# Kernel optimization log

Measured on AMD Instinct MI355X. Metric: run time of the kernel, lower is better.

The kernel has to match this reference:

```python
import jax, jax.numpy as jnp
import numpy as np

B, D, DOUT, R, H = 16384, 1024, 1024, 8, 16
DH = D // 2  # route hidden dim


def setup_inputs() -> dict:
    key = jax.random.key(0)
    ks = jax.random.split(key, 12)
    s = 0.02
    return {
        "x": jax.random.normal(ks[0], (B, D), dtype=jnp.float32),
        # nn.MultiheadAttention packed in_proj: [3D, D] (q,k,v stacked)
        "in_proj_w": jax.random.normal(ks[1], (3 * D, D), dtype=jnp.float32) * s,
        "in_proj_b": jax.random.normal(ks[2], (3 * D,), dtype=jnp.float32) * s,
        "out_proj_w": jax.random.normal(ks[3], (D, D), dtype=jnp.float32) * s,
        "out_proj_b": jax.random.normal(ks[4], (D,), dtype=jnp.float32) * s,
        # R expert MLPs, batched: Linear(D, D//2) -> ReLU -> Linear(D//2, DOUT)
        "W1": jax.random.normal(ks[5], (R, DH, D), dtype=jnp.float32) * s,
        "b1": jax.random.normal(ks[6], (R, DH), dtype=jnp.float32) * s,
        "W2": jax.random.normal(ks[7], (R, DOUT, DH), dtype=jnp.float32) * s,
        "b2": jax.random.normal(ks[8], (R, DOUT), dtype=jnp.float32) * s,
        # gate: Linear(D, R) + softmax
        "Wg": jax.random.normal(ks[9], (R, D), dtype=jnp.float32) * s,
        "bg": jax.random.normal(ks[10], (R,), dtype=jnp.float32) * s,
    }


def reference(x, in_proj_w, in_proj_b, out_proj_w, out_proj_b, W1, b1, W2, b2, Wg, bg):
    # --- MultiheadAttention over seq_len == 1 ---
    # softmax over a single key position is exactly 1 (for every head),
    # so attn_output == V; the Q/K projections provably do not affect the
    # output or any gradient (d softmax(single logit) = 0). Hence only the
    # V slice of the packed in_proj and the output projection matter.
    Wv = in_proj_w[2 * D:]          # [D, D]
    bv = in_proj_b[2 * D:]          # [D]
    v = x @ Wv.T + bv               # [B, D]
    attended = v @ out_proj_w.T + out_proj_b  # [B, D]

    # --- R small expert MLPs as one batched/grouped GEMM (dropout in eval mode = identity) ---
    h = jax.nn.relu(jnp.einsum('bd,rhd->brh', attended, W1) + b1)   # [B, R, DH]
    route_out = jnp.einsum('brh,roh->bro', h, W2) + b2              # [B, R, DOUT]

    # --- softmax gate over routes, computed from the ORIGINAL x ---
    gate = jax.nn.softmax(x @ Wg.T + bg, axis=-1)                   # [B, R]

    # gate-weighted sum over routes
    return jnp.einsum('bro,br->bo', route_out, gate)                # [B, DOUT]
```

## Files before the change

### kernel.cpp

```cpp
#include <hip/hip_runtime.h>
#include <hip/hip_bf16.h>
#include <cstdint>

typedef __hip_bfloat16 bf16;
typedef __attribute__((ext_vector_type(8))) short bfrag;
typedef __attribute__((ext_vector_type(4))) float facc;

#define B_    16384
#define D_    1024
#define DOUT_ 1024
#define R_    8
#define DH_   512
#define RH_   4096

#define BM 256
#define BN 256
#define BK 64

#define NXCD 8

#define AS1(p) ((const __attribute__((address_space(1))) void*)(p))
#define AS3(p) ((__attribute__((address_space(3))) void*)(p))

#define DSR(dst, addr, off) \
    asm volatile("ds_read_b128 %0, %1 offset:%c2" : "=v"(dst) : "v"(addr), "i"(off))

static __device__ __forceinline__ uint32_t pack2bf(float a, float b) {
    unsigned short ua = __builtin_bit_cast(unsigned short, __float2bfloat16(a));
    unsigned short ub = __builtin_bit_cast(unsigned short, __float2bfloat16(b));
    return (uint32_t)ua | ((uint32_t)ub << 16);
}

__global__ void k_cvt(const float* __restrict__ in, bf16* __restrict__ out, long n)
{
    long i = ((long)blockIdx.x * blockDim.x + threadIdx.x) * 4;
    if (i >= n) return;
    float4 v = *reinterpret_cast<const float4*>(in + i);
    uint2 o;
    o.x = pack2bf(v.x, v.y);
    o.y = pack2bf(v.z, v.w);
    *reinterpret_cast<uint2*>(out + i) = o;
}

__global__ void k_cvt_w2(const float* __restrict__ W2, bf16* __restrict__ out)
{
    int b = blockIdx.x;
    int r = b >> 10;
    int o = b & 1023;
    const float4* src = reinterpret_cast<const float4*>(W2 + ((long)r * DOUT_ + o) * DH_);
    bf16* dst = out + (long)o * RH_ + r * DH_;
    int t = threadIdx.x;
    float4 v = src[t];
    uint2 p;
    p.x = pack2bf(v.x, v.y);
    p.y = pack2bf(v.z, v.w);
    *reinterpret_cast<uint2*>(dst + t * 4) = p;
}

__global__ __launch_bounds__(256) void k_gate(const float* __restrict__ x,
                                              const float* __restrict__ Wg,
                                              const float* __restrict__ bg,
                                              float* __restrict__ gate)
{
    __shared__ float sWg[R_ * D_];
    __shared__ float sbg[R_];
    for (int i = threadIdx.x; i < R_ * D_ / 4; i += 256)
        reinterpret_cast<float4*>(sWg)[i] = reinterpret_cast<const float4*>(Wg)[i];
    if (threadIdx.x < R_) sbg[threadIdx.x] = bg[threadIdx.x];
    __syncthreads();

    const int lane = threadIdx.x & 63;
    const int wave = threadIdx.x >> 6;
    const int row  = blockIdx.x * 4 + wave;

    const float4* xr = reinterpret_cast<const float4*>(x + (long)row * D_);
    float s[R_] = {};
    #pragma unroll
    for (int c = 0; c < 4; ++c) {
        float4 xv = xr[lane + c * 64];
        #pragma unroll
        for (int r = 0; r < R_; ++r) {
            float4 wv = reinterpret_cast<const float4*>(sWg + r * D_)[lane + c * 64];
            s[r] += xv.x * wv.x + xv.y * wv.y + xv.z * wv.z + xv.w * wv.w;
        }
    }
    #pragma unroll
    for (int r = 0; r < R_; ++r) {
        float v = s[r];
        #pragma unroll
        for (int off = 32; off > 0; off >>= 1) v += __shfl_xor(v, off);
        s[r] = v + sbg[r];
    }
    float m = s[0];
    #pragma unroll
    for (int r = 1; r < R_; ++r) m = fmaxf(m, s[r]);
    float den = 0.f;
    #pragma unroll
    for (int r = 0; r < R_; ++r) { s[r] = __expf(s[r] - m); den += s[r]; }
    float inv = 1.f / den;
    if (lane < R_) gate[(long)row * R_ + lane] = s[lane] * inv;
}

#define MFMA_BF16 __builtin_amdgcn_mfma_f32_16x16x32_bf16

template <int EPI>
__global__ __launch_bounds__(512, 2)
void k_gemm(const bf16* __restrict__ A, const bf16* __restrict__ Bm,
            const float* __restrict__ bias, const float* __restrict__ gate,
            const float* __restrict__ b2v, void* __restrict__ Cout,
            int M, int N, int K, int gate_row0)
{
    __shared__ char lds[131072];

    const int tid  = threadIdx.x;
    const int lane = tid & 63;
    const int wave = tid >> 6;
    const int wr   = wave >> 2;
    const int wc   = wave & 3;

    const int nwg  = gridDim.x * gridDim.y;
    const int orig = blockIdx.y * gridDim.x + blockIdx.x;
    const int xcd  = orig % NXCD;
    const int q    = nwg / NXCD;
    const int rr   = nwg % NXCD;
    const int wgid = (xcd < rr ? xcd * (q + 1) : rr * (q + 1) + (xcd - rr) * q)
                   + orig / NXCD;
    const int bn0  = (wgid % gridDim.x) * BN;
    const int bm0  = (wgid / gridDim.x) * BM;

    const int lrow = lane & 15;
    const int kgrp = lane >> 4;

    const int s_colb  = ((tid & 7) * 16) ^ (((tid >> 3) & 7) << 4);
    const int s_row   = tid >> 3;
    const int lds_off = tid * 16;

    const long Kb   = (long)K * 2;
    const long r64  = 64 * Kb;
    const long r128 = 128 * Kb;
    const char* gA0 = (const char*)A  + (long)(bm0 + s_row) * Kb + s_colb;
    const char* gB0 = (const char*)Bm + (long)(bn0 + s_row) * Kb + s_colb;

    auto stageH = [&](int buf, int h, long kb) {
        char* ldst = lds + buf * 65536
                   + (h < 2 ? h * 16384 : 32768 + (h - 2) * 16384) + lds_off;
        const char* g = (h < 2 ? gA0 + h * r128 : gB0 + (h - 2) * r128) + kb;
        __builtin_amdgcn_global_load_lds(AS1(g),       AS3(ldst),        16, 0, 0);
        __builtin_amdgcn_global_load_lds(AS1(g + r64), AS3(ldst + 8192), 16, 0, 0);
    };

    const int swzk  = (lrow & 7) << 4;
    const int colK0 = (kgrp * 16) ^ swzk;
    const int colK1 = (kgrp * 16 + 64) ^ swzk;
    const uint32_t ldsbase = (uint32_t)(uintptr_t)AS3(lds);
    const uint32_t aA00 = ldsbase + (wr * 128 + lrow) * 128 + colK0;
    const uint32_t aA01 = ldsbase + (wr * 128 + lrow) * 128 + colK1;
    const uint32_t aB00 = ldsbase + 32768 + (wc * 64 + lrow) * 128 + colK0;
    const uint32_t aB01 = ldsbase + 32768 + (wc * 64 + lrow) * 128 + colK1;
    const uint32_t aA10 = aA00 + 65536, aA11 = aA01 + 65536;
    const uint32_t aB10 = aB00 + 65536, aB11 = aB01 + 65536;

    facc acc[8][4];
    #pragma unroll
    for (int m = 0; m < 8; ++m)
        #pragma unroll
        for (int n = 0; n < 4; ++n)
            acc[m][n] = facc{0.f, 0.f, 0.f, 0.f};

    const int NT = K / BK;

    stageH(0, 0, 0); stageH(0, 1, 0); stageH(0, 2, 0); stageH(0, 3, 0);
    stageH(1, 0, 128); stageH(1, 1, 128);
    asm volatile("s_waitcnt vmcnt(4)" ::: "memory");
    __builtin_amdgcn_s_barrier();

    bfrag aF[4][2], bLo[2][2], bHi[2][2];

    auto ktile = [&](int t, uint32_t A0, uint32_t A1, uint32_t Bb0, uint32_t Bb1,
                     int curbuf) {
        const int  nbuf = curbuf ^ 1;
        const long k1b  = (long)(t + 1) * 128;
        const long k2b  = (long)(t + 2) * 128;

        #pragma unroll
        for (int m = 0; m < 4; ++m) {
            DSR(aF[m][0], A0, m * 2048);
            DSR(aF[m][1], A1, m * 2048);
        }
        #pragma unroll
        for (int n = 0; n < 2; ++n) {
            DSR(bLo[n][0], Bb0, n * 2048);
            DSR(bLo[n][1], Bb1, n * 2048);
        }
        if (t + 1 < NT) stageH(nbuf, 2, k1b);
        __builtin_amdgcn_s_barrier();
        asm volatile("s_waitcnt lgkmcnt(0)" ::: "memory");
        __builtin_amdgcn_sched_barrier(0);
        __builtin_amdgcn_s_setprio(1);
        #pragma unroll
        for (int m = 0; m < 4; ++m)
            #pragma unroll
            for (int n = 0; n < 2; ++n) {
                acc[m][n] = MFMA_BF16(aF[m][0], bLo[n][0], acc[m][n], 0, 0, 0);
                acc[m][n] = MFMA_BF16(aF[m][1], bLo[n][1], acc[m][n], 0, 0, 0);
            }
        __builtin_amdgcn_s_setprio(0);
        __builtin_amdgcn_s_barrier();

        #pragma unroll
        for (int n = 0; n < 2; ++n) {
            DSR(bHi[n][0], Bb0, (2 + n) * 2048);
            DSR(bHi[n][1], Bb1, (2 + n) * 2048);
        }
        if (t + 1 < NT) stageH(nbuf, 3, k1b);
        __builtin_amdgcn_s_barrier();
        asm volatile("s_waitcnt lgkmcnt(0)" ::: "memory");
        __builtin_amdgcn_sched_barrier(0);
        __builtin_amdgcn_s_setprio(1);
        #pragma unroll
        for (int m = 0; m < 4; ++m)
            #pragma unroll
            for (int n = 0; n < 2; ++n) {
                acc[m][n + 2] = MFMA_BF16(aF[m][0], bHi[n][0], acc[m][n + 2], 0, 0, 0);
                acc[m][n + 2] = MFMA_BF16(aF[m][1], bHi[n][1], acc[m][n + 2], 0, 0, 0);
            }
        __builtin_amdgcn_s_setprio(0);
        __builtin_amdgcn_s_barrier();

        #pragma unroll
        for (int m = 0; m < 4; ++m) {
            DSR(aF[m][0], A0, (4 + m) * 2048);
            DSR(aF[m][1], A1, (4 + m) * 2048);
        }
        __builtin_amdgcn_s_barrier();
        asm volatile("s_waitcnt lgkmcnt(0)" ::: "memory");
        __builtin_amdgcn_sched_barrier(0);
        __builtin_amdgcn_s_setprio(1);
        #pragma unroll
        for (int m = 0; m < 4; ++m)
            #pragma unroll
            for (int n = 0; n < 2; ++n) {
                acc[m + 4][n + 2] = MFMA_BF16(aF[m][0], bHi[n][0], acc[m + 4][n + 2], 0, 0, 0);
                acc[m + 4][n + 2] = MFMA_BF16(aF[m][1], bHi[n][1], acc[m + 4][n + 2], 0, 0, 0);
            }
        __builtin_amdgcn_s_setprio(0);
        __builtin_amdgcn_s_barrier();

        if (t + 2 < NT) { stageH(curbuf, 0, k2b); stageH(curbuf, 1, k2b); }
        __builtin_amdgcn_s_barrier();
        __builtin_amdgcn_s_setprio(1);
        #pragma unroll
        for (int m = 0; m < 4; ++m)
            #pragma unroll
            for (int n = 0; n < 2; ++n) {
                acc[m + 4][n] = MFMA_BF16(aF[m][0], bLo[n][0], acc[m + 4][n], 0, 0, 0);
                acc[m + 4][n] = MFMA_BF16(aF[m][1], bLo[n][1], acc[m + 4][n], 0, 0, 0);
            }
        __builtin_amdgcn_s_setprio(0);
        if (t + 2 < NT)      asm volatile("s_waitcnt vmcnt(4)" ::: "memory");
        else if (t + 1 < NT) asm volatile("s_waitcnt vmcnt(0)" ::: "memory");
        __builtin_amdgcn_s_barrier();
    };

    for (int t = 0; t < NT; t += 2) {
        ktile(t,     aA00, aA01, aB00, aB01, 0);
        ktile(t + 1, aA10, aA11, aB10, aB11, 1);
    }

    if constexpr (EPI == 2) {
        float* Cf = reinterpret_cast<float*>(Cout);
        float b2c[4][R_];
        #pragma unroll
        for (int n = 0; n < 4; ++n) {
            const int col = bn0 + wc * 64 + n * 16 + lrow;
            #pragma unroll
            for (int r = 0; r < R_; ++r) b2c[n][r] = b2v[r * N + col];
        }
        #pragma unroll
        for (int m = 0; m < 8; ++m) {
            #pragma unroll
            for (int j = 0; j < 4; ++j) {
                const int row = bm0 + wr * 128 + m * 16 + kgrp * 4 + j;
                const float* g = gate + (long)(gate_row0 + row) * R_;
                float gv[R_];
                #pragma unroll
                for (int r = 0; r < R_; ++r) gv[r] = g[r];
                #pragma unroll
                for (int n = 0; n < 4; ++n) {
                    const int col = bn0 + wc * 64 + n * 16 + lrow;
                    float sv = acc[m][n][j];
                    #pragma unroll
                    for (int r = 0; r < R_; ++r) sv += gv[r] * b2c[n][r];
                    Cf[(long)row * N + col] = sv;
                }
            }
        }
    } else {
        bf16* Cb = reinterpret_cast<bf16*>(Cout);
        float bcol[4];
        #pragma unroll
        for (int n = 0; n < 4; ++n) bcol[n] = bias[bn0 + wc * 64 + n * 16 + lrow];
        #pragma unroll
        for (int m = 0; m < 8; ++m) {
            #pragma unroll
            for (int j = 0; j < 4; ++j) {
                const int row = bm0 + wr * 128 + m * 16 + kgrp * 4 + j;
                float gv[4];
                if constexpr (EPI == 1) {
                    #pragma unroll
                    for (int n = 0; n < 4; ++n) {
                        const int col = bn0 + wc * 64 + n * 16 + lrow;
                        gv[n] = gate[(long)(gate_row0 + row) * R_ + (col >> 9)];
                    }
                }
                #pragma unroll
                for (int n = 0; n < 4; ++n) {
                    const int col = bn0 + wc * 64 + n * 16 + lrow;
                    float v = acc[m][n][j] + bcol[n];
                    if constexpr (EPI == 1) v = fmaxf(v, 0.f) * gv[n];
                    Cb[(long)row * N + col] = __float2bfloat16(v);
                }
            }
        }
    }
}

extern "C" void kernel_launch(void* const* d_in, const int* in_sizes, int n_in,
                              void* d_out, int out_size, void* d_ws, size_t ws_size,
                              hipStream_t stream)
{
    const float* x   = (const float*)d_in[0];
    const float* ipw = (const float*)d_in[1];
    const float* ipb = (const float*)d_in[2];
    const float* opw = (const float*)d_in[3];
    const float* opb = (const float*)d_in[4];
    const float* W1  = (const float*)d_in[5];
    const float* b1  = (const float*)d_in[6];
    const float* W2  = (const float*)d_in[7];
    const float* b2  = (const float*)d_in[8];
    const float* Wg  = (const float*)d_in[9];
    const float* bg  = (const float*)d_in[10];
    float* out = (float*)d_out;

    char* ws = (char*)d_ws;
    size_t off = 0;
    auto alloc = [&](size_t bytes) -> void* {
        void* p = ws + off;
        off += (bytes + 255) & ~(size_t)255;
        return p;
    };

    bf16* xb   = (bf16*)alloc((size_t)B_ * D_ * 2);
    bf16* vb   = (bf16*)alloc((size_t)B_ * D_ * 2);
    bf16* Wvb  = (bf16*)alloc((size_t)D_ * D_ * 2);
    bf16* Wob  = (bf16*)alloc((size_t)D_ * D_ * 2);
    bf16* W1b  = (bf16*)alloc((size_t)RH_ * D_ * 2);
    bf16* W2b  = (bf16*)alloc((size_t)DOUT_ * RH_ * 2);
    float* gate = (float*)alloc((size_t)B_ * R_ * 4);

    int mc = B_;
    while (off + (size_t)mc * RH_ * 2 > ws_size && mc > 1024) mc >>= 1;
    bf16* hb = (bf16*)alloc((size_t)mc * RH_ * 2);
    bf16* ab = xb;

    k_cvt<<<(B_ * D_) / 1024, 256, 0, stream>>>(x, xb, (long)B_ * D_);
    k_cvt<<<(D_ * D_) / 1024, 256, 0, stream>>>(ipw + (size_t)2 * D_ * D_, Wvb, (long)D_ * D_);
    k_cvt<<<(D_ * D_) / 1024, 256, 0, stream>>>(opw, Wob, (long)D_ * D_);
    k_cvt<<<(RH_ * D_) / 1024, 256, 0, stream>>>(W1, W1b, (long)RH_ * D_);
    k_cvt_w2<<<R_ * DOUT_, 128, 0, stream>>>(W2, W2b);

    k_gate<<<B_ / 4, 256, 0, stream>>>(x, Wg, bg, gate);

    k_gemm<0><<<dim3(D_ / BN, B_ / BM), 512, 0, stream>>>(
        xb, Wvb, ipb + 2 * D_, nullptr, nullptr, vb, B_, D_, D_, 0);

    k_gemm<0><<<dim3(D_ / BN, B_ / BM), 512, 0, stream>>>(
        vb, Wob, opb, nullptr, nullptr, ab, B_, D_, D_, 0);

    for (int m0 = 0; m0 < B_; m0 += mc) {
        k_gemm<1><<<dim3(RH_ / BN, mc / BM), 512, 0, stream>>>(
            ab + (size_t)m0 * D_, W1b, b1, gate, nullptr, hb, mc, RH_, D_, m0);
        k_gemm<2><<<dim3(DOUT_ / BN, mc / BM), 512, 0, stream>>>(
            hb, W2b, nullptr, gate, b2, out + (size_t)m0 * DOUT_, mc, DOUT_, RH_, m0);
    }
}
```

Before: 385.7 us.

## Software-pipeline LDS fragment reads across k-tiles with double-buffered B fragments

```diff
diff --git a/kernel.cpp b/kernel.cpp
--- a/kernel.cpp
+++ b/kernel.cpp
@@ -169,30 +169,31 @@
 
     const int NT = K / BK;
 
+    bfrag aF[4][2];
+    bfrag bHi[2][2];
+    bfrag bLoE[2][2];
+    bfrag bLoO[2][2];
+
     stageH(0, 0, 0); stageH(0, 1, 0); stageH(0, 2, 0); stageH(0, 3, 0);
     stageH(1, 0, 128); stageH(1, 1, 128);
     asm volatile("s_waitcnt vmcnt(4)" ::: "memory");
     __builtin_amdgcn_s_barrier();
-
-    bfrag aF[4][2], bLo[2][2], bHi[2][2];
-
-    auto ktile = [&](int t, uint32_t A0, uint32_t A1, uint32_t Bb0, uint32_t Bb1,
-                     int curbuf) {
-        const int  nbuf = curbuf ^ 1;
-        const long k1b  = (long)(t + 1) * 128;
-        const long k2b  = (long)(t + 2) * 128;
-
-        #pragma unroll
-        for (int m = 0; m < 4; ++m) {
-            DSR(aF[m][0], A0, m * 2048);
-            DSR(aF[m][1], A1, m * 2048);
-        }
-        #pragma unroll
-        for (int n = 0; n < 2; ++n) {
-            DSR(bLo[n][0], Bb0, n * 2048);
-            DSR(bLo[n][1], Bb1, n * 2048);
-        }
-        if (t + 1 < NT) stageH(nbuf, 2, k1b);
+    #pragma unroll
+    for (int m = 0; m < 4; ++m) { DSR(aF[m][0], aA00, 0 * 2048 + 0); DSR(aF[m][1], aA01, 0); }
+    #pragma unroll
+    for (int m = 0; m < 4; ++m) { DSR(aF[m][0], aA00, m * 2048); DSR(aF[m][1], aA01, m * 2048); }
+    #pragma unroll
+    for (int n = 0; n < 2; ++n) { DSR(bLoE[n][0], aB00, n * 2048); DSR(bLoE[n][1], aB01, n * 2048); }
+
+    auto ktile = [&](int t, int curbuf,
+                     uint32_t A0c, uint32_t A1c, uint32_t B0c, uint32_t B1c,
+                     uint32_t A0n, uint32_t A1n, uint32_t B0n, uint32_t B1n,
+                     bfrag (&bLoC)[2][2], bfrag (&bLoN)[2][2]) {
+        const long k1b = (long)(t + 1) * 128;
+        const long k2b = (long)(t + 2) * 128;
+        const int  nb  = curbuf ^ 1;
+
+        if (t + 1 < NT) stageH(nb, 2, k1b);
         __builtin_amdgcn_s_barrier();
         asm volatile("s_waitcnt lgkmcnt(0)" ::: "memory");
         __builtin_amdgcn_sched_barrier(0);
@@ -201,18 +202,18 @@
         for (int m = 0; m < 4; ++m)
             #pragma unroll
             for (int n = 0; n < 2; ++n) {
-                acc[m][n] = MFMA_BF16(aF[m][0], bLo[n][0], acc[m][n], 0, 0, 0);
-                acc[m][n] = MFMA_BF16(aF[m][1], bLo[n][1], acc[m][n], 0, 0, 0);
+                acc[m][n] = MFMA_BF16(aF[m][0], bLoC[n][0], acc[m][n], 0, 0, 0);
+                acc[m][n] = MFMA_BF16(aF[m][1], bLoC[n][1], acc[m][n], 0, 0, 0);
             }
         __builtin_amdgcn_s_setprio(0);
-        __builtin_amdgcn_s_barrier();
-
         #pragma unroll
         for (int n = 0; n < 2; ++n) {
-            DSR(bHi[n][0], Bb0, (2 + n) * 2048);
-            DSR(bHi[n][1], Bb1, (2 + n) * 2048);
-        }
-        if (t + 1 < NT) stageH(nbuf, 3, k1b);
+            DSR(bHi[n][0], B0c, (2 + n) * 2048);
+            DSR(bHi[n][1], B1c, (2 + n) * 2048);
+        }
+        __builtin_amdgcn_s_barrier();
+
+        if (t + 1 < NT) stageH(nb, 3, k1b);
         __builtin_amdgcn_s_barrier();
         asm volatile("s_waitcnt lgkmcnt(0)" ::: "memory");
         __builtin_amdgcn_sched_barrier(0);
@@ -225,13 +226,14 @@
                 acc[m][n + 2] = MFMA_BF16(aF[m][1], bHi[n][1], acc[m][n + 2], 0, 0, 0);
             }
         __builtin_amdgcn_s_setprio(0);
-        __builtin_amdgcn_s_barrier();
-
         #pragma unroll
         for (int m = 0; m < 4; ++m) {
-            DSR(aF[m][0], A0, (4 + m) * 2048);
-            DSR(aF[m][1], A1, (4 + m) * 2048);
-        }
+            DSR(aF[m][0], A0c, (4 + m) * 2048);
+            DSR(aF[m][1], A1c, (4 + m) * 2048);
+        }
+        __builtin_amdgcn_s_barrier();
+
+        if (t + 2 < NT) stageH(curbuf, 0, k2b);
         __builtin_amdgcn_s_barrier();
         asm volatile("s_waitcnt lgkmcnt(0)" ::: "memory");
         __builtin_amdgcn_sched_barrier(0);
@@ -246,25 +248,42 @@
         __builtin_amdgcn_s_setprio(0);
         __builtin_amdgcn_s_barrier();
 
-        if (t + 2 < NT) { stageH(curbuf, 0, k2b); stageH(curbuf, 1, k2b); }
-        __builtin_amdgcn_s_barrier();
+        if (t + 2 < NT) {
+            stageH(curbuf, 1, k2b);
+            asm volatile("s_waitcnt vmcnt(4)" ::: "memory");
+        } else if (t + 1 < NT) {
+            asm volatile("s_waitcnt vmcnt(0)" ::: "memory");
+        }
+        __builtin_amdgcn_s_barrier();
+        asm volatile("s_waitcnt lgkmcnt(0)" ::: "memory");
+        __builtin_amdgcn_sched_barrier(0);
         __builtin_amdgcn_s_setprio(1);
         #pragma unroll
         for (int m = 0; m < 4; ++m)
             #pragma unroll
             for (int n = 0; n < 2; ++n) {
-                acc[m + 4][n] = MFMA_BF16(aF[m][0], bLo[n][0], acc[m + 4][n], 0, 0, 0);
-                acc[m + 4][n] = MFMA_BF16(aF[m][1], bLo[n][1], acc[m + 4][n], 0, 0, 0);
+                acc[m + 4][n] = MFMA_BF16(aF[m][0], bLoC[n][0], acc[m + 4][n], 0, 0, 0);
+                acc[m + 4][n] = MFMA_BF16(aF[m][1], bLoC[n][1], acc[m + 4][n], 0, 0, 0);
             }
         __builtin_amdgcn_s_setprio(0);
-        if (t + 2 < NT)      asm volatile("s_waitcnt vmcnt(4)" ::: "memory");
-        else if (t + 1 < NT) asm volatile("s_waitcnt vmcnt(0)" ::: "memory");
+        if (t + 1 < NT) {
+            #pragma unroll
+            for (int m = 0; m < 4; ++m) {
+                DSR(aF[m][0], A0n, m * 2048);
+                DSR(aF[m][1], A1n, m * 2048);
+            }
+            #pragma unroll
+            for (int n = 0; n < 2; ++n) {
+                DSR(bLoN[n][0], B0n, n * 2048);
+                DSR(bLoN[n][1], B1n, n * 2048);
+            }
+        }
         __builtin_amdgcn_s_barrier();
     };
 
     for (int t = 0; t < NT; t += 2) {
-        ktile(t,     aA00, aA01, aB00, aB01, 0);
-        ktile(t + 1, aA10, aA11, aB10, aB11, 1);
+        ktile(t,     0, aA00, aA01, aB00, aB01, aA10, aA11, aB10, aB11, bLoE, bLoO);
+        ktile(t + 1, 1, aA10, aA11, aB10, aB11, aA00, aA01, aB00, aB01, bLoO, bLoE);
     }
 
     if constexpr (EPI == 2) {
```

Measured after the change: 388.2 us. About the same (+0.6%).
